# Kernel optimization log

Hardware: AMD Instinct MI355X
Metric: run time of the kernel (lower is better)

The kernel has to match this reference:

```python
import jax, jax.numpy as jnp
import numpy as np

K = 2  # active_experts (top-k)


def setup_inputs() -> dict:
    key = jax.random.key(0)
    ks = jax.random.split(key, 7)
    B, S, D, E = 2, 2048, 1024, 8
    H = 4 * D
    sd = 1.0 / np.sqrt(D)
    sh = 1.0 / np.sqrt(H)
    return {
        "x": jax.random.normal(ks[0], (B, S, D), jnp.float32),
        "Wr": jax.random.normal(ks[1], (D, E), jnp.float32) * sd,
        "br": jax.random.normal(ks[2], (E,), jnp.float32) * sd,
        "W1": jax.random.normal(ks[3], (E, D, H), jnp.float32) * sd,
        "b1": jax.random.normal(ks[4], (E, H), jnp.float32) * sd,
        "W2": jax.random.normal(ks[5], (E, H, D), jnp.float32) * sh,
        "b2": jax.random.normal(ks[6], (E, D), jnp.float32) * sh,
    }


def reference(x, Wr, br, W1, b1, W2, b2):
    E = Wr.shape[-1]
    # Router: top-k gating with softmax over only the selected experts.
    scores = jnp.einsum("bsd,de->bse", x, Wr) + br            # [B,S,E]
    _, topk_idx = jax.lax.top_k(scores, K)                     # [B,S,K]
    indicator = jax.nn.one_hot(topk_idx, E, dtype=scores.dtype).sum(-2)  # [B,S,E] 0/1
    neg_inf = jnp.asarray(-jnp.inf, scores.dtype)
    weights = jax.nn.softmax(jnp.where(indicator > 0, scores, neg_inf), axis=-1)

    # Dense masked expert loop (faithful to the original module's math).
    out = jnp.zeros_like(x)
    for i in range(E):
        xi = x * indicator[..., i:i + 1]                       # masked inputs
        h = jax.nn.relu(jnp.einsum("bsd,dh->bsh", xi, W1[i]) + b1[i])
        yi = jnp.einsum("bsh,hd->bsd", h, W2[i]) + b2[i]
        out = out + yi * weights[..., i:i + 1]
    return out
```

## Files before the change

kernel.cpp:

```cpp
#include <hip/hip_runtime.h>
#include <math.h>

#define T_TOKENS 4096
#define D_DIM    1024
#define E_EXP    8
#define H_DIM    4096
#define NSLOT    8192
#define NSLOTP   (NSLOT + 128)
#define MAXTILE  72

#define LDSTRIDE 40

typedef __attribute__((ext_vector_type(8))) short   short8;
typedef __attribute__((ext_vector_type(4))) float   floatx4;

__device__ __forceinline__ unsigned short f2bf(float f) {
    unsigned int u = __float_as_uint(f);
    u += 0x7fffu + ((u >> 16) & 1u);
    return (unsigned short)(u >> 16);
}
__device__ __forceinline__ short8 pack8(const float4 a, const float4 b) {
    short8 r;
    r[0] = (short)f2bf(a.x); r[1] = (short)f2bf(a.y);
    r[2] = (short)f2bf(a.z); r[3] = (short)f2bf(a.w);
    r[4] = (short)f2bf(b.x); r[5] = (short)f2bf(b.y);
    r[6] = (short)f2bf(b.z); r[7] = (short)f2bf(b.w);
    return r;
}

typedef __attribute__((address_space(1))) const unsigned int guint;
typedef __attribute__((address_space(3))) unsigned int luint;
__device__ __forceinline__ void gl_lds16(const void* g, void* l) {
    __builtin_amdgcn_global_load_lds((guint*)g, (luint*)l, 16, 0, 0);
}

__global__ __launch_bounds__(256)
void moe_router_kernel(const float* __restrict__ x,
                       const float* __restrict__ Wr,
                       const float* __restrict__ br,
                       const float* __restrict__ b2,
                       float* __restrict__ out,
                       int* __restrict__ counts,
                       int* __restrict__ tok_id,
                       float* __restrict__ tok_w)
{
    const int token = blockIdx.x * 4 + (threadIdx.x >> 6);
    const int lane  = threadIdx.x & 63;

    float s[E_EXP];
#pragma unroll
    for (int e = 0; e < E_EXP; e++) s[e] = 0.0f;

    const float* xrow = x + (size_t)token * D_DIM;
#pragma unroll
    for (int i = 0; i < D_DIM / 64; i++) {
        int d = lane + 64 * i;
        float xv = xrow[d];
        const float4* wr4 = (const float4*)(Wr + (size_t)d * E_EXP);
        float4 w0 = wr4[0], w1 = wr4[1];
        s[0] = fmaf(xv, w0.x, s[0]); s[1] = fmaf(xv, w0.y, s[1]);
        s[2] = fmaf(xv, w0.z, s[2]); s[3] = fmaf(xv, w0.w, s[3]);
        s[4] = fmaf(xv, w1.x, s[4]); s[5] = fmaf(xv, w1.y, s[5]);
        s[6] = fmaf(xv, w1.z, s[6]); s[7] = fmaf(xv, w1.w, s[7]);
    }
#pragma unroll
    for (int off = 32; off >= 1; off >>= 1) {
#pragma unroll
        for (int e = 0; e < E_EXP; e++) s[e] += __shfl_xor(s[e], off, 64);
    }
#pragma unroll
    for (int e = 0; e < E_EXP; e++) s[e] += br[e];

    int e0 = 0; float v0 = s[0];
#pragma unroll
    for (int e = 1; e < E_EXP; e++) if (s[e] > v0) { v0 = s[e]; e0 = e; }
    int e1 = (e0 == 0) ? 1 : 0; float v1 = s[e1];
#pragma unroll
    for (int e = 0; e < E_EXP; e++)
        if (e != e0 && s[e] > v1) { v1 = s[e]; e1 = e; }

    float p1 = __expf(v1 - v0);
    float inv = 1.0f / (1.0f + p1);
    float w0 = inv, w1 = p1 * inv;

    if (lane == 0) {
        int slot0 = atomicAdd(&counts[e0], 1);
        tok_id[e0 * T_TOKENS + slot0] = token;
        tok_w [e0 * T_TOKENS + slot0] = w0;
        int slot1 = atomicAdd(&counts[e1], 1);
        tok_id[e1 * T_TOKENS + slot1] = token;
        tok_w [e1 * T_TOKENS + slot1] = w1;
    }

    float* orow = out + (size_t)token * D_DIM;
    const float* b20 = b2 + (size_t)e0 * D_DIM;
    const float* b21 = b2 + (size_t)e1 * D_DIM;
#pragma unroll
    for (int i = 0; i < D_DIM / 64; i++) {
        int d = lane + 64 * i;
        orow[d] = fmaf(w0, b20[d], w1 * b21[d]);
    }
}

__global__ void moe_scan_kernel(const int* __restrict__ counts,
                                int* __restrict__ offs,
                                int* __restrict__ ntiles,
                                int* __restrict__ tiles)
{
    if (threadIdx.x == 0) {
        int a = 0, nt = 0;
#pragma unroll
        for (int e = 0; e < E_EXP; e++) {
            offs[e] = a;
            int m = (counts[e] + 127) >> 7;
            for (int t = 0; t < m; t++) tiles[nt++] = (e << 16) | t;
            a += counts[e];
        }
        *ntiles = nt;
    }
}


__device__ __forceinline__ void wstage_body(const float* __restrict__ M,
                                            unsigned short* __restrict__ S,
                                            int R, int C, int bx, int by, int e)
{
    __shared__ unsigned short T[64 * 72];
    const float* Me = M + (size_t)e * R * C;
    unsigned short* Se = S + (size_t)e * R * C;
    const int c0 = bx * 64, r0 = by * 64;
    const int tid = threadIdx.x;
    const int rl = tid >> 2, cc = (tid & 3) * 16;

    const float* src = Me + (size_t)(r0 + rl) * C + c0 + cc;
#pragma unroll
    for (int j = 0; j < 4; j++) {
        float4 v = *(const float4*)(src + 4 * j);
        T[(cc + 4 * j + 0) * 72 + rl] = f2bf(v.x);
        T[(cc + 4 * j + 1) * 72 + rl] = f2bf(v.y);
        T[(cc + 4 * j + 2) * 72 + rl] = f2bf(v.z);
        T[(cc + 4 * j + 3) * 72 + rl] = f2bf(v.w);
    }
    __syncthreads();
#pragma unroll
    for (int it = 0; it < 2; it++) {
        int cell = tid + 256 * it;
        int c = cell & 63, g = cell >> 6;
        short8 v = *(const short8*)&T[c * 72 + g * 8];
        *(short8*)&Se[(((size_t)(r0 >> 3) + g) * C + c0 + c) * 8] = v;
    }
}

__device__ __forceinline__ void xgather_body(const float* __restrict__ x,
                                             const int* __restrict__ offs,
                                             const int* __restrict__ tok_id,
                                             unsigned short* __restrict__ Xg,
                                             int bx)
{
    const int gslot = (bx & 31) * 256 + threadIdx.x;
    int e = 0;
#pragma unroll
    for (int i = 1; i < E_EXP; i++) if (gslot >= offs[i]) e = i;
    const int loc = gslot - offs[e];
    const int token = tok_id[e * T_TOKENS + loc];
    const float* xr = x + (size_t)token * D_DIM;
    const int g0 = (bx >> 5) * 16;
#pragma unroll
    for (int g = g0; g < g0 + 16; g++) {
        float4 v0 = *(const float4*)(xr + g * 8);
        float4 v1 = *(const float4*)(xr + g * 8 + 4);
        *(short8*)&Xg[((size_t)g * NSLOTP + gslot) * 8] = pack8(v0, v1);
    }
}

__global__ __launch_bounds__(256)
void moe_wstage_kernel(const float* __restrict__ M, unsigned short* __restrict__ S,
                       int R, int C)
{
    wstage_body(M, S, R, C, blockIdx.x, blockIdx.y, blockIdx.z);
}

__global__ __launch_bounds__(256)
void moe_xgather_kernel(const float* __restrict__ x, const int* __restrict__ offs,
                        const int* __restrict__ tok_id, unsigned short* __restrict__ Xg)
{
    xgather_body(x, offs, tok_id, Xg, blockIdx.y * 32 + blockIdx.x);
}

__global__ __launch_bounds__(256)
void moe_stage_all(const float* __restrict__ x,
                   const float* __restrict__ W1,
                   const float* __restrict__ W2,
                   const int* __restrict__ offs,
                   const int* __restrict__ tok_id,
                   unsigned short* __restrict__ Xg,
                   unsigned short* __restrict__ W1S,
                   unsigned short* __restrict__ W2S)
{
    const int bid = blockIdx.x;
    if (bid < 8192) {
        wstage_body(W1, W1S, D_DIM, H_DIM, bid & 63, (bid >> 6) & 15, bid >> 10);
    } else if (bid < 16384) {
        int id = bid - 8192;
        wstage_body(W2, W2S, H_DIM, D_DIM, id & 15, (id >> 4) & 63, id >> 10);
    } else {
        xgather_body(x, offs, tok_id, Xg, bid - 16384);
    }
}


__global__ __launch_bounds__(256, 4)
void moe_ffn1_fast(const unsigned short* __restrict__ Xg,
                   const unsigned short* __restrict__ W1S,
                   const float* __restrict__ b1,
                   const int* __restrict__ counts,
                   const int* __restrict__ offs,
                   const float* __restrict__ tok_w,
                   const int* __restrict__ ntiles,
                   const int* __restrict__ tiles,
                   unsigned short* __restrict__ Hbuf)
{
    const int ty = blockIdx.y;
    if (ty >= *ntiles) return;
    const int pk  = tiles[ty];
    const int e   = pk >> 16;
    const int m0  = (pk & 0xffff) << 7;
    const int n_e = counts[e];
    const int h0  = blockIdx.x * 128;
    const int hb  = offs[e];
    const int tid  = threadIdx.x;
    const int lane = tid & 63;
    const int wave = tid >> 6;
    const int wy = (wave >> 1) * 64, wx = (wave & 1) * 64;
    const int ml = lane & 15, q = lane >> 4;

    __shared__ unsigned short As[8 * 128 * 8];
    __shared__ unsigned short Bs[8 * 128 * 8];
    __shared__ float wts_s[128];
    __shared__ float b1s[128];

    if (tid < 128) {
        int slot = m0 + tid;
        wts_s[tid] = (slot < n_e) ? tok_w[e * T_TOKENS + slot] : 0.0f;
        b1s[tid]   = b1[(size_t)e * H_DIM + h0 + tid];
    }

    floatx4 zero = {0.f, 0.f, 0.f, 0.f};
    floatx4 acc[4][4];
#pragma unroll
    for (int i = 0; i < 4; i++)
#pragma unroll
        for (int j = 0; j < 4; j++) acc[i][j] = zero;

    const unsigned short* Be = W1S + (size_t)e * D_DIM * H_DIM;
    const size_t arow = (size_t)(hb + m0);

    for (int kk8 = 0; kk8 < D_DIM / 8; kk8 += 8) {
#pragma unroll
        for (int t = 0; t < 4; t++) {
            int cbase = (t * 4 + wave) * 64;
            int c = cbase + lane;
            int g = c >> 7, r = c & 127;
            gl_lds16(&Xg[((size_t)(kk8 + g) * NSLOTP + arow + r) * 8], &As[cbase * 8]);
            gl_lds16(&Be[((size_t)(kk8 + g) * H_DIM + h0 + r) * 8],    &Bs[cbase * 8]);
        }
        __syncthreads();
#pragma unroll
        for (int ks = 0; ks < 2; ks++) {
            short8 a[4], b[4];
#pragma unroll
            for (int i = 0; i < 4; i++)
                a[i] = *(const short8*)&As[(((ks * 4 + q) * 128) + wy + i * 16 + ml) * 8];
#pragma unroll
            for (int j = 0; j < 4; j++)
                b[j] = *(const short8*)&Bs[(((ks * 4 + q) * 128) + wx + j * 16 + ml) * 8];
#pragma unroll
            for (int i = 0; i < 4; i++)
#pragma unroll
                for (int j = 0; j < 4; j++)
                    acc[i][j] = __builtin_amdgcn_mfma_f32_16x16x32_bf16(
                                    a[i], b[j], acc[i][j], 0, 0, 0);
        }
        __syncthreads();
    }

#pragma unroll
    for (int i = 0; i < 4; i++) {
#pragma unroll
        for (int r = 0; r < 4; r++) {
            int row  = wy + i * 16 + q * 4 + r;
            int slot = m0 + row;
            if (slot < n_e) {
                float w = wts_s[row];
                int gslot = hb + slot;
#pragma unroll
                for (int j = 0; j < 4; j++) {
                    int hcol = h0 + wx + j * 16 + ml;
                    float v = fmaxf(acc[i][j][r] + b1s[wx + j * 16 + ml], 0.0f) * w;
                    Hbuf[((size_t)(hcol >> 3) * NSLOTP + gslot) * 8 + (hcol & 7)] = f2bf(v);
                }
            }
        }
    }
}

__global__ __launch_bounds__(256, 4)
void moe_ffn2_fast(const unsigned short* __restrict__ Hbuf,
                   const unsigned short* __restrict__ W2S,
                   float* __restrict__ out,
                   const int* __restrict__ counts,
                   const int* __restrict__ offs,
                   const int* __restrict__ tok_id,
                   const int* __restrict__ ntiles,
                   const int* __restrict__ tiles)
{
    const int ty = blockIdx.y;
    if (ty >= *ntiles) return;
    const int pk  = tiles[ty];
    const int e   = pk >> 16;
    const int m0  = (pk & 0xffff) << 7;
    const int n_e = counts[e];
    const int d0  = (blockIdx.x & 7) * 128;
    const int kb  = (blockIdx.x >> 3) * (H_DIM / 8 / 2);
    const int hb  = offs[e];
    const int tid  = threadIdx.x;
    const int lane = tid & 63;
    const int wave = tid >> 6;
    const int wy = (wave >> 1) * 64, wx = (wave & 1) * 64;
    const int ml = lane & 15, q = lane >> 4;

    __shared__ unsigned short As[8 * 128 * 8];
    __shared__ unsigned short Bs[8 * 128 * 8];
    __shared__ int ids_s[128];

    if (tid < 128) {
        int slot = m0 + tid;
        ids_s[tid] = (slot < n_e) ? tok_id[e * T_TOKENS + slot] : 0;
    }

    floatx4 zero = {0.f, 0.f, 0.f, 0.f};
    floatx4 acc[4][4];
#pragma unroll
    for (int i = 0; i < 4; i++)
#pragma unroll
        for (int j = 0; j < 4; j++) acc[i][j] = zero;

    const unsigned short* Be = W2S + (size_t)e * H_DIM * D_DIM;
    const size_t arow = (size_t)(hb + m0);

    for (int kk8 = kb; kk8 < kb + H_DIM / 8 / 2; kk8 += 8) {
#pragma unroll
        for (int t = 0; t < 4; t++) {
            int cbase = (t * 4 + wave) * 64;
            int c = cbase + lane;
            int g = c >> 7, r = c & 127;
            gl_lds16(&Hbuf[((size_t)(kk8 + g) * NSLOTP + arow + r) * 8], &As[cbase * 8]);
            gl_lds16(&Be[((size_t)(kk8 + g) * D_DIM + d0 + r) * 8],      &Bs[cbase * 8]);
        }
        __syncthreads();
#pragma unroll
        for (int ks = 0; ks < 2; ks++) {
            short8 a[4], b[4];
#pragma unroll
            for (int i = 0; i < 4; i++)
                a[i] = *(const short8*)&As[(((ks * 4 + q) * 128) + wy + i * 16 + ml) * 8];
#pragma unroll
            for (int j = 0; j < 4; j++)
                b[j] = *(const short8*)&Bs[(((ks * 4 + q) * 128) + wx + j * 16 + ml) * 8];
#pragma unroll
            for (int i = 0; i < 4; i++)
#pragma unroll
                for (int j = 0; j < 4; j++)
                    acc[i][j] = __builtin_amdgcn_mfma_f32_16x16x32_bf16(
                                    a[i], b[j], acc[i][j], 0, 0, 0);
        }
        __syncthreads();
    }

#pragma unroll
    for (int i = 0; i < 4; i++) {
#pragma unroll
        for (int r = 0; r < 4; r++) {
            int row  = wy + i * 16 + q * 4 + r;
            int slot = m0 + row;
            if (slot < n_e) {
                float* orow = out + (size_t)ids_s[row] * D_DIM + d0 + wx;
#pragma unroll
                for (int j = 0; j < 4; j++)
                    atomicAdd(&orow[j * 16 + ml], acc[i][j][r]);
            }
        }
    }
}


__global__ __launch_bounds__(256, 2)
void moe_ffn1_kernel(const float* __restrict__ x,
                     const float* __restrict__ W1,
                     const float* __restrict__ b1,
                     const int* __restrict__ counts,
                     const int* __restrict__ offs,
                     const int* __restrict__ tok_id,
                     const float* __restrict__ tok_w,
                     unsigned short* __restrict__ Hbuf)
{
    const int e   = blockIdx.z;
    const int n_e = counts[e];
    const int m0  = blockIdx.y * 128;
    if (m0 >= n_e) return;
    const int h0  = blockIdx.x * 128;
    const int hb  = offs[e];
    const int tid  = threadIdx.x;
    const int lane = tid & 63;
    const int wave = tid >> 6;
    const int wy = (wave >> 1) * 64;
    const int wx = (wave & 1) * 64;
    const int ml = lane & 15;
    const int q  = lane >> 4;

    __shared__ unsigned short xs[128 * LDSTRIDE];
    __shared__ unsigned short wt[128 * LDSTRIDE];
    __shared__ int   ids_s[128];
    __shared__ float wts_s[128];
    __shared__ float b1s[128];

    if (tid < 128) {
        int slot = m0 + tid;
        ids_s[tid] = (slot < n_e) ? tok_id[e * T_TOKENS + slot] : 0;
        wts_s[tid] = (slot < n_e) ? tok_w[e * T_TOKENS + slot] : 0.0f;
        b1s[tid]   = b1[(size_t)e * H_DIM + h0 + tid];
    }
    __syncthreads();

    floatx4 zero = {0.f, 0.f, 0.f, 0.f};
    floatx4 acc[4][4];
#pragma unroll
    for (int i = 0; i < 4; i++)
#pragma unroll
        for (int j = 0; j < 4; j++) acc[i][j] = zero;

    const float* W1e = W1 + (size_t)e * D_DIM * H_DIM + h0;
    const int xr = tid >> 1;
    const int xc = (tid & 1) * 16;
    const int wc = tid & 31;
    const int wk = tid >> 5;
    const size_t xrow_base = (size_t)ids_s[xr] * D_DIM;

    for (int kk = 0; kk < D_DIM; kk += 32) {
        {
            const float* src = x + xrow_base + kk + xc;
            unsigned short* dst = &xs[xr * LDSTRIDE + xc];
#pragma unroll
            for (int i = 0; i < 4; i++) {
                float4 v = *(const float4*)(src + 4 * i);
                ushort4 o = make_ushort4(f2bf(v.x), f2bf(v.y), f2bf(v.z), f2bf(v.w));
                *(ushort4*)(dst + 4 * i) = o;
            }
        }
#pragma unroll
        for (int it = 0; it < 4; it++) {
            int k = wk + 8 * it;
            const float* src = W1e + (size_t)(kk + k) * H_DIM + wc;
#pragma unroll
            for (int j = 0; j < 4; j++)
                wt[(wc + 32 * j) * LDSTRIDE + k] = f2bf(src[32 * j]);
        }
        __syncthreads();

        short8 a[4], b[4];
#pragma unroll
        for (int i = 0; i < 4; i++)
            a[i] = *(const short8*)&xs[(wy + i * 16 + ml) * LDSTRIDE + q * 8];
#pragma unroll
        for (int j = 0; j < 4; j++)
            b[j] = *(const short8*)&wt[(wx + j * 16 + ml) * LDSTRIDE + q * 8];
#pragma unroll
        for (int i = 0; i < 4; i++)
#pragma unroll
            for (int j = 0; j < 4; j++)
                acc[i][j] = __builtin_amdgcn_mfma_f32_16x16x32_bf16(
                                a[i], b[j], acc[i][j], 0, 0, 0);
        __syncthreads();
    }

#pragma unroll
    for (int i = 0; i < 4; i++) {
#pragma unroll
        for (int r = 0; r < 4; r++) {
            int row  = wy + i * 16 + q * 4 + r;
            int slot = m0 + row;
            if (slot < n_e) {
                float w = wts_s[row];
                size_t base = (size_t)(hb + slot) * H_DIM + h0 + wx;
#pragma unroll
                for (int j = 0; j < 4; j++) {
                    float v = acc[i][j][r] + b1s[wx + j * 16 + ml];
                    v = fmaxf(v, 0.0f) * w;
                    Hbuf[base + j * 16 + ml] = f2bf(v);
                }
            }
        }
    }
}

__global__ __launch_bounds__(256, 2)
void moe_ffn2_kernel(const float* __restrict__ W2,
                     float* __restrict__ out,
                     const int* __restrict__ counts,
                     const int* __restrict__ offs,
                     const int* __restrict__ tok_id,
                     const unsigned short* __restrict__ Hbuf)
{
    const int e   = blockIdx.z;
    const int n_e = counts[e];
    const int m0  = blockIdx.y * 128;
    if (m0 >= n_e) return;
    const int d0  = blockIdx.x * 128;
    const int hb  = offs[e];
    const int tid  = threadIdx.x;
    const int lane = tid & 63;
    const int wave = tid >> 6;
    const int wy = (wave >> 1) * 64;
    const int wx = (wave & 1) * 64;
    const int ml = lane & 15;
    const int q  = lane >> 4;

    __shared__ unsigned short hs[128 * LDSTRIDE];
    __shared__ unsigned short wt[128 * LDSTRIDE];
    __shared__ int ids_s[128];

    if (tid < 128) {
        int slot = m0 + tid;
        ids_s[tid] = (slot < n_e) ? tok_id[e * T_TOKENS + slot] : 0;
    }
    __syncthreads();

    floatx4 zero = {0.f, 0.f, 0.f, 0.f};
    floatx4 acc[4][4];
#pragma unroll
    for (int i = 0; i < 4; i++)
#pragma unroll
        for (int j = 0; j < 4; j++) acc[i][j] = zero;

    const float* W2e = W2 + (size_t)e * H_DIM * D_DIM + d0;
    const int xr = tid >> 1;
    const int xc = (tid & 1) * 16;
    const int wc = tid & 31;
    const int wk = tid >> 5;
    const int hrow = min(hb + m0 + xr, NSLOT - 1);
    const size_t hrow_base = (size_t)hrow * H_DIM;

    for (int kk = 0; kk < H_DIM; kk += 32) {
        {
            const unsigned short* src = Hbuf + hrow_base + kk + xc;
            unsigned short* dst = &hs[xr * LDSTRIDE + xc];
#pragma unroll
            for (int i = 0; i < 4; i++)
                *(ushort4*)(dst + 4 * i) = *(const ushort4*)(src + 4 * i);
        }
#pragma unroll
        for (int it = 0; it < 4; it++) {
            int k = wk + 8 * it;
            const float* src = W2e + (size_t)(kk + k) * D_DIM + wc;
#pragma unroll
            for (int j = 0; j < 4; j++)
                wt[(wc + 32 * j) * LDSTRIDE + k] = f2bf(src[32 * j]);
        }
        __syncthreads();

        short8 a[4], b[4];
#pragma unroll
        for (int i = 0; i < 4; i++)
            a[i] = *(const short8*)&hs[(wy + i * 16 + ml) * LDSTRIDE + q * 8];
#pragma unroll
        for (int j = 0; j < 4; j++)
            b[j] = *(const short8*)&wt[(wx + j * 16 + ml) * LDSTRIDE + q * 8];
#pragma unroll
        for (int i = 0; i < 4; i++)
#pragma unroll
            for (int j = 0; j < 4; j++)
                acc[i][j] = __builtin_amdgcn_mfma_f32_16x16x32_bf16(
                                a[i], b[j], acc[i][j], 0, 0, 0);
        __syncthreads();
    }

#pragma unroll
    for (int i = 0; i < 4; i++) {
#pragma unroll
        for (int r = 0; r < 4; r++) {
            int row  = wy + i * 16 + q * 4 + r;
            int slot = m0 + row;
            if (slot < n_e) {
                float* orow = out + (size_t)ids_s[row] * D_DIM + d0 + wx;
#pragma unroll
                for (int j = 0; j < 4; j++)
                    atomicAdd(&orow[j * 16 + ml], acc[i][j][r]);
            }
        }
    }
}


extern "C" void kernel_launch(void* const* d_in, const int* in_sizes, int n_in,
                              void* d_out, int out_size, void* d_ws, size_t ws_size,
                              hipStream_t stream) {
    const float* x  = (const float*)d_in[0];
    const float* Wr = (const float*)d_in[1];
    const float* br = (const float*)d_in[2];
    const float* W1 = (const float*)d_in[3];
    const float* b1 = (const float*)d_in[4];
    const float* W2 = (const float*)d_in[5];
    const float* b2 = (const float*)d_in[6];
    float* out = (float*)d_out;

    int*   counts = (int*)d_ws;
    int*   offs   = (int*)((char*)d_ws + 64);
    int*   ntiles = (int*)((char*)d_ws + 128);
    int*   tiles  = (int*)((char*)d_ws + 192);
    int*   tok_id = (int*)((char*)d_ws + 4096);
    float* tok_w  = (float*)((char*)d_ws + 4096 + E_EXP * T_TOKENS * 4);

    const size_t OFF_XG  = 1u << 20;
    const size_t SZ_XG   = (size_t)(D_DIM / 8) * NSLOTP * 16;
    const size_t OFF_W1  = OFF_XG + SZ_XG;
    const size_t SZ_W    = (size_t)E_EXP * D_DIM * H_DIM * 2;
    const size_t SZ_HB   = (size_t)(H_DIM / 8) * NSLOTP * 16;
    const size_t OFF_HB_A  = OFF_W1 + SZ_W;
    const size_t NEED_FAST = OFF_HB_A + SZ_HB;
    const size_t OFF_W2    = OFF_W1 + SZ_W;
    const size_t OFF_HB_B  = OFF_W2 + SZ_W;
    const size_t NEED_BIG  = OFF_HB_B + SZ_HB;

    hipMemsetAsync(d_ws, 0, 64, stream);

    moe_router_kernel<<<T_TOKENS / 4, 256, 0, stream>>>(
        x, Wr, br, b2, out, counts, tok_id, tok_w);
    moe_scan_kernel<<<1, 64, 0, stream>>>(counts, offs, ntiles, tiles);

    if (ws_size >= NEED_BIG) {
        unsigned short* Xg   = (unsigned short*)((char*)d_ws + OFF_XG);
        unsigned short* W1S  = (unsigned short*)((char*)d_ws + OFF_W1);
        unsigned short* W2S  = (unsigned short*)((char*)d_ws + OFF_W2);
        unsigned short* Hbuf = (unsigned short*)((char*)d_ws + OFF_HB_B);

        moe_stage_all<<<16384 + 256, 256, 0, stream>>>(
            x, W1, W2, offs, tok_id, Xg, W1S, W2S);

        moe_ffn1_fast<<<dim3(H_DIM / 128, MAXTILE), 256, 0, stream>>>(
            Xg, W1S, b1, counts, offs, tok_w, ntiles, tiles, Hbuf);

        moe_ffn2_fast<<<dim3(16, MAXTILE), 256, 0, stream>>>(
            Hbuf, W2S, out, counts, offs, tok_id, ntiles, tiles);
    } else if (ws_size >= NEED_FAST) {
        unsigned short* Xg   = (unsigned short*)((char*)d_ws + OFF_XG);
        unsigned short* Wsh  = (unsigned short*)((char*)d_ws + OFF_W1);
        unsigned short* Hbuf = (unsigned short*)((char*)d_ws + OFF_HB_A);

        moe_xgather_kernel<<<dim3(32, 8), 256, 0, stream>>>(x, offs, tok_id, Xg);
        moe_wstage_kernel<<<dim3(H_DIM / 64, D_DIM / 64, E_EXP), 256, 0, stream>>>(
            W1, Wsh, D_DIM, H_DIM);
        moe_ffn1_fast<<<dim3(H_DIM / 128, MAXTILE), 256, 0, stream>>>(
            Xg, Wsh, b1, counts, offs, tok_w, ntiles, tiles, Hbuf);
        moe_wstage_kernel<<<dim3(D_DIM / 64, H_DIM / 64, E_EXP), 256, 0, stream>>>(
            W2, Wsh, H_DIM, D_DIM);
        moe_ffn2_fast<<<dim3(16, MAXTILE), 256, 0, stream>>>(
            Hbuf, Wsh, out, counts, offs, tok_id, ntiles, tiles);
    } else {
        unsigned short* Hbuf = (unsigned short*)((char*)d_ws + 524288);

        dim3 g1(H_DIM / 128, T_TOKENS / 128, E_EXP);
        moe_ffn1_kernel<<<g1, 256, 0, stream>>>(
            x, W1, b1, counts, offs, tok_id, tok_w, Hbuf);

        dim3 g2(D_DIM / 128, T_TOKENS / 128, E_EXP);
        moe_ffn2_kernel<<<g2, 256, 0, stream>>>(
            W2, out, counts, offs, tok_id, Hbuf);
    }
}
```

Before: 653.9 us.

## Fuse x bf16 conversion into router, gather rows in FFN1, use 256-row tiles

```diff
diff --git a/kernel.cpp b/kernel.cpp
--- a/kernel.cpp
+++ b/kernel.cpp
@@ -6,8 +6,8 @@
 #define E_EXP    8
 #define H_DIM    4096
 #define NSLOT    8192
-#define NSLOTP   (NSLOT + 128)
-#define MAXTILE  72
+#define NSLOTP   (NSLOT + 256)
+#define MAXT256  40
 
 #define LDSTRIDE 40
 
@@ -18,14 +18,6 @@
     unsigned int u = __float_as_uint(f);
     u += 0x7fffu + ((u >> 16) & 1u);
     return (unsigned short)(u >> 16);
-}
-__device__ __forceinline__ short8 pack8(const float4 a, const float4 b) {
-    short8 r;
-    r[0] = (short)f2bf(a.x); r[1] = (short)f2bf(a.y);
-    r[2] = (short)f2bf(a.z); r[3] = (short)f2bf(a.w);
-    r[4] = (short)f2bf(b.x); r[5] = (short)f2bf(b.y);
-    r[6] = (short)f2bf(b.z); r[7] = (short)f2bf(b.w);
-    return r;
 }
 
 typedef __attribute__((address_space(1))) const unsigned int guint;
@@ -42,7 +34,8 @@
                        float* __restrict__ out,
                        int* __restrict__ counts,
                        int* __restrict__ tok_id,
-                       float* __restrict__ tok_w)
+                       float* __restrict__ tok_w,
+                       unsigned short* __restrict__ xbf)
 {
     const int token = blockIdx.x * 4 + (threadIdx.x >> 6);
     const int lane  = threadIdx.x & 63;
@@ -52,17 +45,22 @@
     for (int e = 0; e < E_EXP; e++) s[e] = 0.0f;
 
     const float* xrow = x + (size_t)token * D_DIM;
+    float xv[16];
 #pragma unroll
     for (int i = 0; i < D_DIM / 64; i++) {
         int d = lane + 64 * i;
-        float xv = xrow[d];
+        xv[i] = xrow[d];
         const float4* wr4 = (const float4*)(Wr + (size_t)d * E_EXP);
         float4 w0 = wr4[0], w1 = wr4[1];
-        s[0] = fmaf(xv, w0.x, s[0]); s[1] = fmaf(xv, w0.y, s[1]);
-        s[2] = fmaf(xv, w0.z, s[2]); s[3] = fmaf(xv, w0.w, s[3]);
-        s[4] = fmaf(xv, w1.x, s[4]); s[5] = fmaf(xv, w1.y, s[5]);
-        s[6] = fmaf(xv, w1.z, s[6]); s[7] = fmaf(xv, w1.w, s[7]);
-    }
+        s[0] = fmaf(xv[i], w0.x, s[0]); s[1] = fmaf(xv[i], w0.y, s[1]);
+        s[2] = fmaf(xv[i], w0.z, s[2]); s[3] = fmaf(xv[i], w0.w, s[3]);
+        s[4] = fmaf(xv[i], w1.x, s[4]); s[5] = fmaf(xv[i], w1.y, s[5]);
+        s[6] = fmaf(xv[i], w1.z, s[6]); s[7] = fmaf(xv[i], w1.w, s[7]);
+    }
+    unsigned short* xb = xbf + (size_t)token * D_DIM;
+#pragma unroll
+    for (int i = 0; i < D_DIM / 64; i++) xb[lane + 64 * i] = f2bf(xv[i]);
+
 #pragma unroll
     for (int off = 32; off >= 1; off >>= 1) {
 #pragma unroll
@@ -112,14 +110,13 @@
 #pragma unroll
         for (int e = 0; e < E_EXP; e++) {
             offs[e] = a;
-            int m = (counts[e] + 127) >> 7;
+            int m = (counts[e] + 255) >> 8;
             for (int t = 0; t < m; t++) tiles[nt++] = (e << 16) | t;
             a += counts[e];
         }
         *ntiles = nt;
     }
 }
-
 
 __device__ __forceinline__ void wstage_body(const float* __restrict__ M,
                                             unsigned short* __restrict__ S,
@@ -151,28 +148,6 @@
     }
 }
 
-__device__ __forceinline__ void xgather_body(const float* __restrict__ x,
-                                             const int* __restrict__ offs,
-                                             const int* __restrict__ tok_id,
-                                             unsigned short* __restrict__ Xg,
-                                             int bx)
-{
-    const int gslot = (bx & 31) * 256 + threadIdx.x;
-    int e = 0;
-#pragma unroll
-    for (int i = 1; i < E_EXP; i++) if (gslot >= offs[i]) e = i;
-    const int loc = gslot - offs[e];
-    const int token = tok_id[e * T_TOKENS + loc];
-    const float* xr = x + (size_t)token * D_DIM;
-    const int g0 = (bx >> 5) * 16;
-#pragma unroll
-    for (int g = g0; g < g0 + 16; g++) {
-        float4 v0 = *(const float4*)(xr + g * 8);
-        float4 v1 = *(const float4*)(xr + g * 8 + 4);
-        *(short8*)&Xg[((size_t)g * NSLOTP + gslot) * 8] = pack8(v0, v1);
-    }
-}
-
 __global__ __launch_bounds__(256)
 void moe_wstage_kernel(const float* __restrict__ M, unsigned short* __restrict__ S,
                        int R, int C)
@@ -181,103 +156,95 @@
 }
 
 __global__ __launch_bounds__(256)
-void moe_xgather_kernel(const float* __restrict__ x, const int* __restrict__ offs,
-                        const int* __restrict__ tok_id, unsigned short* __restrict__ Xg)
-{
-    xgather_body(x, offs, tok_id, Xg, blockIdx.y * 32 + blockIdx.x);
-}
-
-__global__ __launch_bounds__(256)
-void moe_stage_all(const float* __restrict__ x,
-                   const float* __restrict__ W1,
+void moe_stage_all(const float* __restrict__ W1,
                    const float* __restrict__ W2,
-                   const int* __restrict__ offs,
-                   const int* __restrict__ tok_id,
-                   unsigned short* __restrict__ Xg,
                    unsigned short* __restrict__ W1S,
                    unsigned short* __restrict__ W2S)
 {
     const int bid = blockIdx.x;
     if (bid < 8192) {
         wstage_body(W1, W1S, D_DIM, H_DIM, bid & 63, (bid >> 6) & 15, bid >> 10);
-    } else if (bid < 16384) {
+    } else {
         int id = bid - 8192;
         wstage_body(W2, W2S, H_DIM, D_DIM, id & 15, (id >> 4) & 63, id >> 10);
-    } else {
-        xgather_body(x, offs, tok_id, Xg, bid - 16384);
-    }
-}
-
-
-__global__ __launch_bounds__(256, 4)
-void moe_ffn1_fast(const unsigned short* __restrict__ Xg,
+    }
+}
+
+
+__global__ __launch_bounds__(256, 2)
+void moe_ffn1_fast(const unsigned short* __restrict__ xbf,
                    const unsigned short* __restrict__ W1S,
                    const float* __restrict__ b1,
                    const int* __restrict__ counts,
                    const int* __restrict__ offs,
+                   const int* __restrict__ tok_id,
                    const float* __restrict__ tok_w,
                    const int* __restrict__ ntiles,
                    const int* __restrict__ tiles,
                    unsigned short* __restrict__ Hbuf)
 {
-    const int ty = blockIdx.y;
-    if (ty >= *ntiles) return;
-    const int pk  = tiles[ty];
+    const int tx = blockIdx.x;
+    if (tx >= *ntiles) return;
+    const int pk  = tiles[tx];
     const int e   = pk >> 16;
-    const int m0  = (pk & 0xffff) << 7;
+    const int m0  = (pk & 0xffff) << 8;
     const int n_e = counts[e];
-    const int h0  = blockIdx.x * 128;
+    const int h0  = blockIdx.y * 128;
     const int hb  = offs[e];
     const int tid  = threadIdx.x;
     const int lane = tid & 63;
     const int wave = tid >> 6;
-    const int wy = (wave >> 1) * 64, wx = (wave & 1) * 64;
+    const int wy = wave * 64;
     const int ml = lane & 15, q = lane >> 4;
 
-    __shared__ unsigned short As[8 * 128 * 8];
+    __shared__ unsigned short As[8 * 256 * 8];
     __shared__ unsigned short Bs[8 * 128 * 8];
-    __shared__ float wts_s[128];
+    __shared__ float wts_s[256];
     __shared__ float b1s[128];
 
-    if (tid < 128) {
+    {
         int slot = m0 + tid;
         wts_s[tid] = (slot < n_e) ? tok_w[e * T_TOKENS + slot] : 0.0f;
-        b1s[tid]   = b1[(size_t)e * H_DIM + h0 + tid];
-    }
+        if (tid < 128) b1s[tid] = b1[(size_t)e * H_DIM + h0 + tid];
+    }
+
+    int aslot = m0 + tid;
+    int atok  = (aslot < n_e) ? tok_id[e * T_TOKENS + aslot] : 0;
+    const unsigned short* abase = xbf + (size_t)atok * D_DIM;
 
     floatx4 zero = {0.f, 0.f, 0.f, 0.f};
-    floatx4 acc[4][4];
+    floatx4 acc[4][8];
 #pragma unroll
     for (int i = 0; i < 4; i++)
 #pragma unroll
-        for (int j = 0; j < 4; j++) acc[i][j] = zero;
+        for (int j = 0; j < 8; j++) acc[i][j] = zero;
 
     const unsigned short* Be = W1S + (size_t)e * D_DIM * H_DIM;
-    const size_t arow = (size_t)(hb + m0);
+    const int br_ = tid & 127;
+    const int bg_ = tid >> 7;
 
     for (int kk8 = 0; kk8 < D_DIM / 8; kk8 += 8) {
 #pragma unroll
-        for (int t = 0; t < 4; t++) {
-            int cbase = (t * 4 + wave) * 64;
-            int c = cbase + lane;
-            int g = c >> 7, r = c & 127;
-            gl_lds16(&Xg[((size_t)(kk8 + g) * NSLOTP + arow + r) * 8], &As[cbase * 8]);
-            gl_lds16(&Be[((size_t)(kk8 + g) * H_DIM + h0 + r) * 8],    &Bs[cbase * 8]);
-        }
+        for (int f = 0; f < 8; f++)
+            gl_lds16(abase + (size_t)(kk8 + f) * 8, &As[(f * 256 + wave * 64) * 8]);
+#pragma unroll
+        for (int f = 0; f < 4; f++)
+            gl_lds16(&Be[((size_t)(kk8 + f * 2 + bg_) * H_DIM + h0 + br_) * 8],
+                     &Bs[(f * 256 + wave * 64) * 8]);
         __syncthreads();
 #pragma unroll
         for (int ks = 0; ks < 2; ks++) {
-            short8 a[4], b[4];
+            short8 a[4], b[8];
 #pragma unroll
             for (int i = 0; i < 4; i++)
-                a[i] = *(const short8*)&As[(((ks * 4 + q) * 128) + wy + i * 16 + ml) * 8];
-#pragma unroll
-            for (int j = 0; j < 4; j++)
-                b[j] = *(const short8*)&Bs[(((ks * 4 + q) * 128) + wx + j * 16 + ml) * 8];
+                a[i] = *(const short8*)&As[((ks * 4 + q) * 256 + wy + i * 16 + ml) * 8];
+#pragma unroll
+            for (int j = 0; j < 8; j++)
+                b[j] = *(const short8*)&Bs[((ks * 4 + q) * 128 + j * 16 + ml) * 8];
 #pragma unroll
             for (int i = 0; i < 4; i++)
 #pragma unroll
-                for (int j = 0; j < 4; j++)
+                for (int j = 0; j < 8; j++)
                     acc[i][j] = __builtin_amdgcn_mfma_f32_16x16x32_bf16(
                                     a[i], b[j], acc[i][j], 0, 0, 0);
         }
@@ -294,9 +261,9 @@
                 float w = wts_s[row];
                 int gslot = hb + slot;
 #pragma unroll
-                for (int j = 0; j < 4; j++) {
-                    int hcol = h0 + wx + j * 16 + ml;
-                    float v = fmaxf(acc[i][j][r] + b1s[wx + j * 16 + ml], 0.0f) * w;
+                for (int j = 0; j < 8; j++) {
+                    int hcol = h0 + j * 16 + ml;
+                    float v = fmaxf(acc[i][j][r] + b1s[j * 16 + ml], 0.0f) * w;
                     Hbuf[((size_t)(hcol >> 3) * NSLOTP + gslot) * 8 + (hcol & 7)] = f2bf(v);
                 }
             }
@@ -304,7 +271,7 @@
     }
 }
 
-__global__ __launch_bounds__(256, 4)
+__global__ __launch_bounds__(256, 2)
 void moe_ffn2_fast(const unsigned short* __restrict__ Hbuf,
                    const unsigned short* __restrict__ W2S,
                    float* __restrict__ out,
@@ -314,63 +281,66 @@
                    const int* __restrict__ ntiles,
                    const int* __restrict__ tiles)
 {
-    const int ty = blockIdx.y;
-    if (ty >= *ntiles) return;
-    const int pk  = tiles[ty];
+    const int tx = blockIdx.x;
+    if (tx >= *ntiles) return;
+    const int pk  = tiles[tx];
     const int e   = pk >> 16;
-    const int m0  = (pk & 0xffff) << 7;
+    const int m0  = (pk & 0xffff) << 8;
     const int n_e = counts[e];
-    const int d0  = (blockIdx.x & 7) * 128;
-    const int kb  = (blockIdx.x >> 3) * (H_DIM / 8 / 2);
+    const int d0  = (blockIdx.y & 7) * 128;
+    const int kb  = (blockIdx.y >> 3) * (H_DIM / 8 / 2);
     const int hb  = offs[e];
     const int tid  = threadIdx.x;
     const int lane = tid & 63;
     const int wave = tid >> 6;
-    const int wy = (wave >> 1) * 64, wx = (wave & 1) * 64;
+    const int wy = wave * 64;
     const int ml = lane & 15, q = lane >> 4;
 
-    __shared__ unsigned short As[8 * 128 * 8];
+    __shared__ unsigned short As[8 * 256 * 8];
     __shared__ unsigned short Bs[8 * 128 * 8];
-    __shared__ int ids_s[128];
-
-    if (tid < 128) {
+    __shared__ int ids_s[256];
+
+    {
         int slot = m0 + tid;
         ids_s[tid] = (slot < n_e) ? tok_id[e * T_TOKENS + slot] : 0;
     }
 
     floatx4 zero = {0.f, 0.f, 0.f, 0.f};
-    floatx4 acc[4][4];
+    floatx4 acc[4][8];
 #pragma unroll
     for (int i = 0; i < 4; i++)
 #pragma unroll
-        for (int j = 0; j < 4; j++) acc[i][j] = zero;
+        for (int j = 0; j < 8; j++) acc[i][j] = zero;
 
     const unsigned short* Be = W2S + (size_t)e * H_DIM * D_DIM;
     const size_t arow = (size_t)(hb + m0);
+    const unsigned short* abase = Hbuf + (arow + tid) * 8;
+    const int br_ = tid & 127;
+    const int bg_ = tid >> 7;
 
     for (int kk8 = kb; kk8 < kb + H_DIM / 8 / 2; kk8 += 8) {
 #pragma unroll
-        for (int t = 0; t < 4; t++) {
-            int cbase = (t * 4 + wave) * 64;
-            int c = cbase + lane;
-            int g = c >> 7, r = c & 127;
-            gl_lds16(&Hbuf[((size_t)(kk8 + g) * NSLOTP + arow + r) * 8], &As[cbase * 8]);
-            gl_lds16(&Be[((size_t)(kk8 + g) * D_DIM + d0 + r) * 8],      &Bs[cbase * 8]);
-        }
+        for (int f = 0; f < 8; f++)
+            gl_lds16(abase + (size_t)(kk8 + f) * NSLOTP * 8,
+                     &As[(f * 256 + wave * 64) * 8]);
+#pragma unroll
+        for (int f = 0; f < 4; f++)
+            gl_lds16(&Be[((size_t)(kk8 + f * 2 + bg_) * D_DIM + d0 + br_) * 8],
+                     &Bs[(f * 256 + wave * 64) * 8]);
         __syncthreads();
 #pragma unroll
         for (int ks = 0; ks < 2; ks++) {
-            short8 a[4], b[4];
+            short8 a[4], b[8];
 #pragma unroll
             for (int i = 0; i < 4; i++)
-                a[i] = *(const short8*)&As[(((ks * 4 + q) * 128) + wy + i * 16 + ml) * 8];
-#pragma unroll
-            for (int j = 0; j < 4; j++)
-                b[j] = *(const short8*)&Bs[(((ks * 4 + q) * 128) + wx + j * 16 + ml) * 8];
+                a[i] = *(const short8*)&As[((ks * 4 + q) * 256 + wy + i * 16 + ml) * 8];
+#pragma unroll
+            for (int j = 0; j < 8; j++)
+                b[j] = *(const short8*)&Bs[((ks * 4 + q) * 128 + j * 16 + ml) * 8];
 #pragma unroll
             for (int i = 0; i < 4; i++)
 #pragma unroll
-                for (int j = 0; j < 4; j++)
+                for (int j = 0; j < 8; j++)
                     acc[i][j] = __builtin_amdgcn_mfma_f32_16x16x32_bf16(
                                     a[i], b[j], acc[i][j], 0, 0, 0);
         }
@@ -384,9 +354,9 @@
             int row  = wy + i * 16 + q * 4 + r;
             int slot = m0 + row;
             if (slot < n_e) {
-                float* orow = out + (size_t)ids_s[row] * D_DIM + d0 + wx;
-#pragma unroll
-                for (int j = 0; j < 4; j++)
+                float* orow = out + (size_t)ids_s[row] * D_DIM + d0;
+#pragma unroll
+                for (int j = 0; j < 8; j++)
                     atomicAdd(&orow[j * 16 + ml], acc[i][j][r]);
             }
         }
@@ -620,9 +590,9 @@
     int*   tok_id = (int*)((char*)d_ws + 4096);
     float* tok_w  = (float*)((char*)d_ws + 4096 + E_EXP * T_TOKENS * 4);
 
-    const size_t OFF_XG  = 1u << 20;
-    const size_t SZ_XG   = (size_t)(D_DIM / 8) * NSLOTP * 16;
-    const size_t OFF_W1  = OFF_XG + SZ_XG;
+    const size_t OFF_XBF = 1u << 20;
+    const size_t SZ_XBF  = (size_t)T_TOKENS * D_DIM * 2;
+    const size_t OFF_W1  = OFF_XBF + SZ_XBF;
     const size_t SZ_W    = (size_t)E_EXP * D_DIM * H_DIM * 2;
     const size_t SZ_HB   = (size_t)(H_DIM / 8) * NSLOTP * 16;
     const size_t OFF_HB_A  = OFF_W1 + SZ_W;
@@ -633,45 +603,45 @@
 
     hipMemsetAsync(d_ws, 0, 64, stream);
 
-    moe_router_kernel<<<T_TOKENS / 4, 256, 0, stream>>>(
-        x, Wr, br, b2, out, counts, tok_id, tok_w);
-    moe_scan_kernel<<<1, 64, 0, stream>>>(counts, offs, ntiles, tiles);
-
-    if (ws_size >= NEED_BIG) {
-        unsigned short* Xg   = (unsigned short*)((char*)d_ws + OFF_XG);
-        unsigned short* W1S  = (unsigned short*)((char*)d_ws + OFF_W1);
-        unsigned short* W2S  = (unsigned short*)((char*)d_ws + OFF_W2);
-        unsigned short* Hbuf = (unsigned short*)((char*)d_ws + OFF_HB_B);
-
-        moe_stage_all<<<16384 + 256, 256, 0, stream>>>(
-            x, W1, W2, offs, tok_id, Xg, W1S, W2S);
-
-        moe_ffn1_fast<<<dim3(H_DIM / 128, MAXTILE), 256, 0, stream>>>(
-            Xg, W1S, b1, counts, offs, tok_w, ntiles, tiles, Hbuf);
-
-        moe_ffn2_fast<<<dim3(16, MAXTILE), 256, 0, stream>>>(
+    if (ws_size >= NEED_FAST) {
+        unsigned short* xbf = (unsigned short*)((char*)d_ws + OFF_XBF);
+        unsigned short* W1S = (unsigned short*)((char*)d_ws + OFF_W1);
+        const bool big = (ws_size >= NEED_BIG);
+        unsigned short* W2S = (unsigned short*)((char*)d_ws + (big ? OFF_W2 : OFF_W1));
+        unsigned short* Hbuf =
+            (unsigned short*)((char*)d_ws + (big ? OFF_HB_B : OFF_HB_A));
+
+        moe_router_kernel<<<T_TOKENS / 4, 256, 0, stream>>>(
+            x, Wr, br, b2, out, counts, tok_id, tok_w, xbf);
+        moe_scan_kernel<<<1, 64, 0, stream>>>(counts, offs, ntiles, tiles);
+
+        if (big) {
+            moe_stage_all<<<16384, 256, 0, stream>>>(W1, W2, W1S, W2S);
+        } else {
+            moe_wstage_kernel<<<dim3(H_DIM / 64, D_DIM / 64, E_EXP), 256, 0, stream>>>(
+                W1, W1S, D_DIM, H_DIM);
+        }
+
+        moe_ffn1_fast<<<dim3(MAXT256, H_DIM / 128), 256, 0, stream>>>(
+            xbf, W1S, b1, counts, offs, tok_id, tok_w, ntiles, tiles, Hbuf);
+
+        if (!big) {
+            moe_wstage_kernel<<<dim3(D_DIM / 64, H_DIM / 64, E_EXP), 256, 0, stream>>>(
+                W2, W2S, H_DIM, D_DIM);
+        }
+
+        moe_ffn2_fast<<<dim3(MAXT256, 16), 256, 0, stream>>>(
             Hbuf, W2S, out, counts, offs, tok_id, ntiles, tiles);
-    } else if (ws_size >= NEED_FAST) {
-        unsigned short* Xg   = (unsigned short*)((char*)d_ws + OFF_XG);
-        unsigned short* Wsh  = (unsigned short*)((char*)d_ws + OFF_W1);
-        unsigned short* Hbuf = (unsigned short*)((char*)d_ws + OFF_HB_A);
-
-        moe_xgather_kernel<<<dim3(32, 8), 256, 0, stream>>>(x, offs, tok_id, Xg);
-        moe_wstage_kernel<<<dim3(H_DIM / 64, D_DIM / 64, E_EXP), 256, 0, stream>>>(
-            W1, Wsh, D_DIM, H_DIM);
-        moe_ffn1_fast<<<dim3(H_DIM / 128, MAXTILE), 256, 0, stream>>>(
-            Xg, Wsh, b1, counts, offs, tok_w, ntiles, tiles, Hbuf);
-        moe_wstage_kernel<<<dim3(D_DIM / 64, H_DIM / 64, E_EXP), 256, 0, stream>>>(
-            W2, Wsh, H_DIM, D_DIM);
-        moe_ffn2_fast<<<dim3(16, MAXTILE), 256, 0, stream>>>(
-            Hbuf, Wsh, out, counts, offs, tok_id, ntiles, tiles);
     } else {
+        unsigned short* xbf = (unsigned short*)((char*)d_ws + OFF_XBF);
+        moe_router_kernel<<<T_TOKENS / 4, 256, 0, stream>>>(
+            x, Wr, br, b2, out, counts, tok_id, tok_w, xbf);
+        moe_scan_kernel<<<1, 64, 0, stream>>>(counts, offs, ntiles, tiles);
+
         unsigned short* Hbuf = (unsigned short*)((char*)d_ws + 524288);
-
         dim3 g1(H_DIM / 128, T_TOKENS / 128, E_EXP);
         moe_ffn1_kernel<<<g1, 256, 0, stream>>>(
             x, W1, b1, counts, offs, tok_id, tok_w, Hbuf);
-
         dim3 g2(D_DIM / 128, T_TOKENS / 128, E_EXP);
         moe_ffn2_kernel<<<g2, 256, 0, stream>>>(
             W2, out, counts, offs, tok_id, Hbuf);
```

New measurement: 720.5 us. 1.1x slower.
